# Optimization experiments

Hardware: AMD Instinct MI355X
Metric: run time of the kernel (lower is better)

## Reference

```python
import jax, jax.numpy as jnp
import numpy as np

N_USERS = 100000
N_MOVIES = 100000
N_EDGES = 1000000
HIDDEN = 128


def setup_inputs() -> dict:
    key = jax.random.key(0)
    k1, k2, k3, k4, k5, k6, k7 = jax.random.split(key, 7)
    user_features = jax.random.normal(k1, (N_USERS, HIDDEN), dtype=jnp.float32)
    movie_features = jax.random.normal(k2, (N_MOVIES, HIDDEN), dtype=jnp.float32)
    src = jax.random.randint(k3, (N_EDGES,), 0, N_USERS, dtype=jnp.int64 if jax.config.jax_enable_x64 else jnp.int32)
    dst = jax.random.randint(k4, (N_EDGES,), 0, N_MOVIES, dtype=jnp.int64 if jax.config.jax_enable_x64 else jnp.int32)
    edge_index = jnp.stack([src, dst], axis=0)
    # Linear(2*HIDDEN, HIDDEN) params, torch-style init (kaiming uniform ~ U(-1/sqrt(fan_in), 1/sqrt(fan_in)))
    b1_bound = 1.0 / np.sqrt(2 * HIDDEN)
    W1 = jax.random.uniform(k5, (2 * HIDDEN, HIDDEN), minval=-b1_bound, maxval=b1_bound, dtype=jnp.float32)
    b1 = jax.random.uniform(k6, (HIDDEN,), minval=-b1_bound, maxval=b1_bound, dtype=jnp.float32)
    b2_bound = 1.0 / np.sqrt(HIDDEN)
    k8, k9 = jax.random.split(k7)
    W2 = jax.random.uniform(k8, (HIDDEN, 1), minval=-b2_bound, maxval=b2_bound, dtype=jnp.float32)
    b2 = jax.random.uniform(k9, (1,), minval=-b2_bound, maxval=b2_bound, dtype=jnp.float32)
    return {"user_features": user_features, "movie_features": movie_features,
            "edge_index": edge_index, "W1": W1, "b1": b1, "W2": W2, "b2": b2}


def reference(user_features, movie_features, edge_index, W1, b1, W2, b2):
    # Gather endpoint features per edge: [E, H] each
    u = user_features[edge_index[0]]
    m = movie_features[edge_index[1]]
    edge_feats = jnp.concatenate([u, m], axis=1)  # [E, 2H]
    h = jax.nn.relu(edge_feats @ W1 + b1)         # [E, H]
    out = h @ W2 + b2                             # [E, 1]
    return out.reshape(-1)
```

## Files before the change

### kernel.cpp

```cpp
#include <hip/hip_runtime.h>
#include <hip/hip_bf16.h>

typedef short s8v __attribute__((ext_vector_type(8)));
typedef float f4v __attribute__((ext_vector_type(4)));

__device__ __forceinline__ unsigned int bfround(float f) {
    unsigned int x = __float_as_uint(f);
    return (x + 0x7fffu + ((x >> 16) & 1u)) >> 16;
}
__device__ __forceinline__ unsigned int pkbf(float x, float y) {
    __hip_bfloat162 h = __float22bfloat162_rn(make_float2(x, y));
    return *(unsigned int*)&h;
}
__device__ __forceinline__ float i8f(unsigned int w, int k) {
    return (float)((int)(signed char)(w >> (8 * k)));
}

__global__ __launch_bounds__(256) void pack_w(const float* __restrict__ W1,
                                              uint4* __restrict__ WF)
{
    const int half = blockIdx.x;
    #pragma unroll
    for (int iter = 0; iter < 8; ++iter) {
        int idx  = iter * 256 + threadIdx.x;
        int lane = idx & 63;
        int t    = (idx >> 6) & 7;
        int c    = idx >> 9;
        int q = lane >> 4, m = lane & 15;
        unsigned int w[4];
        #pragma unroll
        for (int jj = 0; jj < 4; ++jj) {
            float lo = W1[(size_t)(half * 128 + c * 32 + q * 8 + 2 * jj    ) * 128 + t * 16 + m];
            float hi = W1[(size_t)(half * 128 + c * 32 + q * 8 + 2 * jj + 1) * 128 + t * 16 + m];
            w[jj] = bfround(lo) | (bfround(hi) << 16);
        }
        WF[(size_t)half * 2048 + idx] = make_uint4(w[0], w[1], w[2], w[3]);
    }
}

__global__ __launch_bounds__(256, 2) void proj_kernel(
    const float* __restrict__ userf, const float* __restrict__ movief,
    const uint4* __restrict__ WF, const float* __restrict__ b1,
    uint2* __restrict__ Pu, uint2* __restrict__ Pm,
    float* __restrict__ SU, float* __restrict__ SM,
    int ntiles, int bph)
{
    __shared__ uint4 wlds[2048];
    __shared__ uint4 alds[4][512];

    const int half = blockIdx.x >= bph;
    const int bid  = half ? blockIdx.x - bph : blockIdx.x;
    const float* __restrict__ feat = half ? movief : userf;
    uint2* __restrict__ P = half ? Pm : Pu;
    float* __restrict__ S = half ? SM : SU;
    const uint4* __restrict__ wfh = WF + (size_t)half * 2048;

    #pragma unroll
    for (int i = 0; i < 8; ++i)
        wlds[i * 256 + threadIdx.x] = wfh[i * 256 + threadIdx.x];

    const int lane = threadIdx.x & 63;
    const int wv   = threadIdx.x >> 6;
    const int m    = lane & 15;
    const int q    = lane >> 4;

    const int wid = bid * 4 + wv;
    const int nw  = bph * 4;

    float bias_v[8];
    #pragma unroll
    for (int t = 0; t < 8; ++t)
        bias_v[t] = half ? b1[t * 16 + m] : 0.0f;

    const char* gfeat  = (const char*)feat;
    const int   rhalf  = lane >> 5;
    const int   l31x16 = (lane & 31) * 16;

#define ISSUE_ALL(t_) do {                                                     \
        const char* gb_ = gfeat + (size_t)(t_) * 8192;                         \
        _Pragma("unroll")                                                      \
        for (int j_ = 0; j_ < 8; ++j_) {                                       \
            const int r_ = 2 * j_ + rhalf;                                     \
            const size_t so_ = (size_t)r_ * 512 + (size_t)(l31x16 ^ ((r_ & 7) << 4)); \
            __builtin_amdgcn_global_load_lds(                                  \
                (const __attribute__((address_space(1))) void*)(gb_ + so_),    \
                (__attribute__((address_space(3))) void*)&alds[wv][j_ * 64],   \
                16, 0, 0);                                                     \
        }                                                                      \
    } while (0)

    const int swz = m & 7;
#define APULL(c_, h_) alds[wv][m * 32 + (((c_) * 8 + q * 2 + (h_)) ^ swz)]

#define CVT2(p0, p1, dst) do {                                                 \
        uint4 aw_;                                                             \
        const float4 f0_ = *(const float4*)&(p0);                              \
        const float4 f1_ = *(const float4*)&(p1);                              \
        aw_.x = pkbf(f0_.x, f0_.y); aw_.y = pkbf(f0_.z, f0_.w);                \
        aw_.z = pkbf(f1_.x, f1_.y); aw_.w = pkbf(f1_.z, f1_.w);                \
        dst = *(const s8v*)&aw_;                                               \
    } while (0)

#define MFMA_C(c_, afv) do {                                                   \
        _Pragma("unroll")                                                      \
        for (int t_ = 0; t_ < 8; ++t_) {                                       \
            uint4 wf_ = wlds[((c_) * 8 + t_) * 64 + lane];                     \
            acc[t_] = __builtin_amdgcn_mfma_f32_16x16x32_bf16(                 \
                afv, *(const s8v*)&wf_, acc[t_], 0, 0, 0);                     \
        }                                                                      \
    } while (0)

#define WAIT_VM0()   do { asm volatile("s_waitcnt vmcnt(0)" ::: "memory");  \
                          __builtin_amdgcn_sched_barrier(0); } while (0)
#define WAIT_LGKM0() do { asm volatile("s_waitcnt lgkmcnt(0)" ::: "memory"); \
                          __builtin_amdgcn_sched_barrier(0); } while (0)

    int tile = wid;
    if (tile < ntiles) ISSUE_ALL(tile);

    __syncthreads();

    while (tile < ntiles) {
        const int nxt = tile + nw;

        f4v acc[8];
        #pragma unroll
        for (int t = 0; t < 8; ++t)
            acc[t] = (f4v){bias_v[t], bias_v[t], bias_v[t], bias_v[t]};

        WAIT_VM0();
        uint4 p0 = APULL(0, 0), p1 = APULL(0, 1);
        uint4 p2 = APULL(1, 0), p3 = APULL(1, 1);
        uint4 p4 = APULL(2, 0), p5 = APULL(2, 1);
        uint4 p6 = APULL(3, 0), p7 = APULL(3, 1);
        s8v af0, af1, af2, af3;
        CVT2(p0, p1, af0);
        CVT2(p2, p3, af1);
        CVT2(p4, p5, af2);
        CVT2(p6, p7, af3);
        WAIT_LGKM0();
        if (nxt < ntiles) ISSUE_ALL(nxt);

        MFMA_C(0, af0);
        MFMA_C(1, af1);
        MFMA_C(2, af2);
        MFMA_C(3, af3);

        #pragma unroll
        for (int r = 0; r < 4; ++r) {
            float mx = 0.0f;
            #pragma unroll
            for (int t = 0; t < 8; ++t) mx = fmaxf(mx, fabsf(acc[t][r]));
            #pragma unroll
            for (int off = 1; off < 16; off <<= 1)
                mx = fmaxf(mx, __shfl_xor(mx, off, 64));
            float inv = mx > 0.0f ? 127.0f / mx : 0.0f;

            unsigned int lo = 0, hi = 0;
            #pragma unroll
            for (int t = 0; t < 4; ++t) {
                lo |= ((unsigned int)(__float2int_rn(acc[t][r]     * inv) & 0xff)) << (8 * t);
                hi |= ((unsigned int)(__float2int_rn(acc[t + 4][r] * inv) & 0xff)) << (8 * t);
            }
            int row = tile * 16 + q * 4 + r;
            P[(size_t)row * 16 + m] = make_uint2(lo, hi);
            if (m == 0) S[row] = mx * (1.0f / 127.0f);
        }

        tile = nxt;
    }
#undef ISSUE_ALL
#undef APULL
#undef CVT2
#undef MFMA_C
#undef WAIT_VM0
#undef WAIT_LGKM0
}

__global__ __launch_bounds__(256) void edge_kernel(
    const int* __restrict__ src, const int* __restrict__ dst,
    const uint2* __restrict__ Pu, const uint2* __restrict__ Pm,
    const float* __restrict__ SU, const float* __restrict__ SM,
    const float* __restrict__ W2, const float* __restrict__ b2,
    float* __restrict__ out)
{
    const int lane = threadIdx.x & 63;
    const int L    = lane & 15;
    const int g    = lane >> 4;
    const int eg   = (blockIdx.x * 4 + (threadIdx.x >> 6)) * 16 + g * 4;

    float w2v[8];
    #pragma unroll
    for (int j = 0; j < 8; ++j) w2v[j] = W2[j * 16 + L];

    int si[4], di[4];
    #pragma unroll
    for (int i = 0; i < 4; ++i) { si[i] = src[eg + i]; di[i] = dst[eg + i]; }

    uint2 pu[4], pm[4];
    float scu[4], scm[4];
    #pragma unroll
    for (int i = 0; i < 4; ++i) {
        pu[i] = Pu[(size_t)si[i] * 16 + L];
        pm[i] = Pm[(size_t)di[i] * 16 + L];
        scu[i] = SU[si[i]];
        scm[i] = SM[di[i]];
    }

    float res[4];
    #pragma unroll
    for (int i = 0; i < 4; ++i) {
        const unsigned int uw[2] = {pu[i].x, pu[i].y};
        const unsigned int mw[2] = {pm[i].x, pm[i].y};
        float acc = 0.0f;
        #pragma unroll
        for (int v = 0; v < 2; ++v) {
            #pragma unroll
            for (int k = 0; k < 4; ++k) {
                float h = fmaf(scu[i], i8f(uw[v], k), scm[i] * i8f(mw[v], k));
                acc = fmaf(fmaxf(h, 0.0f), w2v[v * 4 + k], acc);
            }
        }
        #pragma unroll
        for (int off = 1; off < 16; off <<= 1)
            acc += __shfl_xor(acc, off, 64);
        res[i] = acc;
    }

    if (L == 0) {
        float bb = b2[0];
        *(float4*)(out + eg) = make_float4(res[0] + bb, res[1] + bb, res[2] + bb, res[3] + bb);
    }
}

extern "C" void kernel_launch(void* const* d_in, const int* in_sizes, int n_in,
                              void* d_out, int out_size, void* d_ws, size_t ws_size,
                              hipStream_t stream) {
    const float* userf  = (const float*)d_in[0];
    const float* movief = (const float*)d_in[1];
    const int*   eidx   = (const int*)d_in[2];
    const float* W1     = (const float*)d_in[3];
    const float* b1     = (const float*)d_in[4];
    const float* W2     = (const float*)d_in[5];
    const float* b2     = (const float*)d_in[6];
    float* out = (float*)d_out;

    const int NU = in_sizes[0] / 128;
    const int NM = in_sizes[1] / 128;
    const int E  = in_sizes[2] / 2;

    uint2* Pu = (uint2*)d_ws;
    uint2* Pm = Pu + (size_t)NU * 16;
    float* SU = (float*)(Pm + (size_t)NM * 16);
    float* SM = SU + NU;
    uint4* WF = (uint4*)(SM + NM);

    const int ntiles = NU / 16;
    const int bph    = 512;

    pack_w<<<2, 256, 0, stream>>>(W1, WF);
    proj_kernel<<<2 * bph, 256, 0, stream>>>(userf, movief, WF, b1, Pu, Pm, SU, SM, ntiles, bph);
    edge_kernel<<<E / 64, 256, 0, stream>>>(eidx, eidx + E, Pu, Pm, SU, SM, W2, b2, out);
}
```

Baseline: 181.5 us.

## Fuse weight packing into projection kernel and process eight edges per lane group

Removes the separate pack_w launch: each projection block now converts W1 to bf16 fragment layout directly into LDS, issuing its first feature tile loads before the conversion so the two overlap. The edge kernel doubles the edges per 16-lane group from four to eight to raise memory-level parallelism for the gathers, and adds a bounds-checked tail path. In exchange every block redoes the W1 conversion (reading 128 KB of W1 from global/L2 per block) and the edge kernel uses more registers.

```diff
diff --git a/kernel.cpp b/kernel.cpp
--- a/kernel.cpp
+++ b/kernel.cpp
@@ -16,31 +16,9 @@
     return (float)((int)(signed char)(w >> (8 * k)));
 }
 
-__global__ __launch_bounds__(256) void pack_w(const float* __restrict__ W1,
-                                              uint4* __restrict__ WF)
-{
-    const int half = blockIdx.x;
-    #pragma unroll
-    for (int iter = 0; iter < 8; ++iter) {
-        int idx  = iter * 256 + threadIdx.x;
-        int lane = idx & 63;
-        int t    = (idx >> 6) & 7;
-        int c    = idx >> 9;
-        int q = lane >> 4, m = lane & 15;
-        unsigned int w[4];
-        #pragma unroll
-        for (int jj = 0; jj < 4; ++jj) {
-            float lo = W1[(size_t)(half * 128 + c * 32 + q * 8 + 2 * jj    ) * 128 + t * 16 + m];
-            float hi = W1[(size_t)(half * 128 + c * 32 + q * 8 + 2 * jj + 1) * 128 + t * 16 + m];
-            w[jj] = bfround(lo) | (bfround(hi) << 16);
-        }
-        WF[(size_t)half * 2048 + idx] = make_uint4(w[0], w[1], w[2], w[3]);
-    }
-}
-
 __global__ __launch_bounds__(256, 2) void proj_kernel(
     const float* __restrict__ userf, const float* __restrict__ movief,
-    const uint4* __restrict__ WF, const float* __restrict__ b1,
+    const float* __restrict__ W1, const float* __restrict__ b1,
     uint2* __restrict__ Pu, uint2* __restrict__ Pm,
     float* __restrict__ SU, float* __restrict__ SM,
     int ntiles, int bph)
@@ -53,11 +31,6 @@
     const float* __restrict__ feat = half ? movief : userf;
     uint2* __restrict__ P = half ? Pm : Pu;
     float* __restrict__ S = half ? SM : SU;
-    const uint4* __restrict__ wfh = WF + (size_t)half * 2048;
-
-    #pragma unroll
-    for (int i = 0; i < 8; ++i)
-        wlds[i * 256 + threadIdx.x] = wfh[i * 256 + threadIdx.x];
 
     const int lane = threadIdx.x & 63;
     const int wv   = threadIdx.x >> 6;
@@ -66,11 +39,6 @@
 
     const int wid = bid * 4 + wv;
     const int nw  = bph * 4;
-
-    float bias_v[8];
-    #pragma unroll
-    for (int t = 0; t < 8; ++t)
-        bias_v[t] = half ? b1[t * 16 + m] : 0.0f;
 
     const char* gfeat  = (const char*)feat;
     const int   rhalf  = lane >> 5;
@@ -89,6 +57,31 @@
         }                                                                      \
     } while (0)
 
+    int tile = wid;
+    if (tile < ntiles) ISSUE_ALL(tile);
+
+    #pragma unroll
+    for (int it = 0; it < 8; ++it) {
+        int idx = it * 256 + threadIdx.x;
+        int l2  = idx & 63;
+        int t2  = (idx >> 6) & 7;
+        int c2  = idx >> 9;
+        int q2 = l2 >> 4, m2 = l2 & 15;
+        unsigned int w[4];
+        #pragma unroll
+        for (int jj = 0; jj < 4; ++jj) {
+            float lo = W1[(size_t)(half * 128 + c2 * 32 + q2 * 8 + 2 * jj    ) * 128 + t2 * 16 + m2];
+            float hi = W1[(size_t)(half * 128 + c2 * 32 + q2 * 8 + 2 * jj + 1) * 128 + t2 * 16 + m2];
+            w[jj] = bfround(lo) | (bfround(hi) << 16);
+        }
+        wlds[idx] = make_uint4(w[0], w[1], w[2], w[3]);
+    }
+
+    float bias_v[8];
+    #pragma unroll
+    for (int t = 0; t < 8; ++t)
+        bias_v[t] = half ? b1[t * 16 + m] : 0.0f;
+
     const int swz = m & 7;
 #define APULL(c_, h_) alds[wv][m * 32 + (((c_) * 8 + q * 2 + (h_)) ^ swz)]
 
@@ -114,9 +107,6 @@
                           __builtin_amdgcn_sched_barrier(0); } while (0)
 #define WAIT_LGKM0() do { asm volatile("s_waitcnt lgkmcnt(0)" ::: "memory"); \
                           __builtin_amdgcn_sched_barrier(0); } while (0)
-
-    int tile = wid;
-    if (tile < ntiles) ISSUE_ALL(tile);
 
     __syncthreads();
 
@@ -182,54 +172,80 @@
     const uint2* __restrict__ Pu, const uint2* __restrict__ Pm,
     const float* __restrict__ SU, const float* __restrict__ SM,
     const float* __restrict__ W2, const float* __restrict__ b2,
-    float* __restrict__ out)
+    float* __restrict__ out, int E)
 {
     const int lane = threadIdx.x & 63;
     const int L    = lane & 15;
     const int g    = lane >> 4;
-    const int eg   = (blockIdx.x * 4 + (threadIdx.x >> 6)) * 16 + g * 4;
+    const int eg   = ((blockIdx.x * 4 + (threadIdx.x >> 6)) * 4 + g) * 8;
 
     float w2v[8];
     #pragma unroll
     for (int j = 0; j < 8; ++j) w2v[j] = W2[j * 16 + L];
 
-    int si[4], di[4];
-    #pragma unroll
-    for (int i = 0; i < 4; ++i) { si[i] = src[eg + i]; di[i] = dst[eg + i]; }
-
-    uint2 pu[4], pm[4];
-    float scu[4], scm[4];
-    #pragma unroll
-    for (int i = 0; i < 4; ++i) {
-        pu[i] = Pu[(size_t)si[i] * 16 + L];
-        pm[i] = Pm[(size_t)di[i] * 16 + L];
-        scu[i] = SU[si[i]];
-        scm[i] = SM[di[i]];
-    }
-
-    float res[4];
-    #pragma unroll
-    for (int i = 0; i < 4; ++i) {
-        const unsigned int uw[2] = {pu[i].x, pu[i].y};
-        const unsigned int mw[2] = {pm[i].x, pm[i].y};
-        float acc = 0.0f;
-        #pragma unroll
-        for (int v = 0; v < 2; ++v) {
-            #pragma unroll
-            for (int k = 0; k < 4; ++k) {
-                float h = fmaf(scu[i], i8f(uw[v], k), scm[i] * i8f(mw[v], k));
-                acc = fmaf(fmaxf(h, 0.0f), w2v[v * 4 + k], acc);
+    if (eg + 8 <= E) {
+        int si[8], di[8];
+        #pragma unroll
+        for (int i = 0; i < 8; ++i) { si[i] = src[eg + i]; di[i] = dst[eg + i]; }
+
+        uint2 pu[8], pm[8];
+        float scu[8], scm[8];
+        #pragma unroll
+        for (int i = 0; i < 8; ++i) {
+            pu[i] = Pu[(size_t)si[i] * 16 + L];
+            pm[i] = Pm[(size_t)di[i] * 16 + L];
+            scu[i] = SU[si[i]];
+            scm[i] = SM[di[i]];
+        }
+
+        float res[8];
+        #pragma unroll
+        for (int i = 0; i < 8; ++i) {
+            const unsigned int uw[2] = {pu[i].x, pu[i].y};
+            const unsigned int mw[2] = {pm[i].x, pm[i].y};
+            float acc = 0.0f;
+            #pragma unroll
+            for (int v = 0; v < 2; ++v) {
+                #pragma unroll
+                for (int k = 0; k < 4; ++k) {
+                    float h = fmaf(scu[i], i8f(uw[v], k), scm[i] * i8f(mw[v], k));
+                    acc = fmaf(fmaxf(h, 0.0f), w2v[v * 4 + k], acc);
+                }
             }
-        }
-        #pragma unroll
-        for (int off = 1; off < 16; off <<= 1)
-            acc += __shfl_xor(acc, off, 64);
-        res[i] = acc;
-    }
-
-    if (L == 0) {
-        float bb = b2[0];
-        *(float4*)(out + eg) = make_float4(res[0] + bb, res[1] + bb, res[2] + bb, res[3] + bb);
+            #pragma unroll
+            for (int off = 1; off < 16; off <<= 1)
+                acc += __shfl_xor(acc, off, 64);
+            res[i] = acc;
+        }
+
+        if (L == 0) {
+            float bb = b2[0];
+            *(float4*)(out + eg)     = make_float4(res[0] + bb, res[1] + bb, res[2] + bb, res[3] + bb);
+            *(float4*)(out + eg + 4) = make_float4(res[4] + bb, res[5] + bb, res[6] + bb, res[7] + bb);
+        }
+    } else if (eg < E) {
+        for (int i = 0; i < 8; ++i) {
+            int e = eg + i;
+            if (e >= E) break;
+            int s = src[e], d = dst[e];
+            uint2 pue = Pu[(size_t)s * 16 + L];
+            uint2 pme = Pm[(size_t)d * 16 + L];
+            float su = SU[s], sm = SM[d];
+            const unsigned int uw[2] = {pue.x, pue.y};
+            const unsigned int mw[2] = {pme.x, pme.y};
+            float acc = 0.0f;
+            #pragma unroll
+            for (int v = 0; v < 2; ++v)
+                #pragma unroll
+                for (int k = 0; k < 4; ++k) {
+                    float h = fmaf(su, i8f(uw[v], k), sm * i8f(mw[v], k));
+                    acc = fmaf(fmaxf(h, 0.0f), w2v[v * 4 + k], acc);
+                }
+            #pragma unroll
+            for (int off = 1; off < 16; off <<= 1)
+                acc += __shfl_xor(acc, off, 64);
+            if (L == 0) out[e] = acc + b2[0];
+        }
     }
 }
 
@@ -253,12 +269,10 @@
     uint2* Pm = Pu + (size_t)NU * 16;
     float* SU = (float*)(Pm + (size_t)NM * 16);
     float* SM = SU + NU;
-    uint4* WF = (uint4*)(SM + NM);
 
     const int ntiles = NU / 16;
     const int bph    = 512;
 
-    pack_w<<<2, 256, 0, stream>>>(W1, WF);
-    proj_kernel<<<2 * bph, 256, 0, stream>>>(userf, movief, WF, b1, Pu, Pm, SU, SM, ntiles, bph);
-    edge_kernel<<<E / 64, 256, 0, stream>>>(eidx, eidx + E, Pu, Pm, SU, SM, W2, b2, out);
-}
+    proj_kernel<<<2 * bph, 256, 0, stream>>>(userf, movief, W1, b1, Pu, Pm, SU, SM, ntiles, bph);
+    edge_kernel<<<(E + 127) / 128, 256, 0, stream>>>(eidx, eidx + E, Pu, Pm, SU, SM, W2, b2, out, E);
+}
```

New measurement: 180.6 us. About the same (-0.5%).
